# Performance work log

Measured on AMD Instinct MI355X. Metric: run time of the kernel, lower is better.

## Reference

```python
import jax, jax.numpy as jnp
import numpy as np

L1 = 513          # max_data_length + 1
EMB = 64          # embedding_dim (w)
V = 6             # num_tokens
B = 128           # batch

def setup_inputs() -> dict:
    key = jax.random.key(0)
    k1, k2, k3 = jax.random.split(key, 3)
    src = jax.random.randint(k1, (B, L1), 0, V, dtype=jnp.int64)
    # nn.Embedding default init: N(0,1)
    embedding = jax.random.normal(k2, (V, EMB), dtype=jnp.float32)
    # xavier_uniform over (L1, EMB, L1, V): fan_in = EMB*L1*V? torch treats dim0 as fan_out... use gain scale ~ sqrt(6/(fan_in+fan_out)) with fan computed on flattened dims
    fan_in = EMB * L1 * V
    fan_out = L1
    bound = float(np.sqrt(6.0 / (fan_in + fan_out)))
    weight = jax.random.uniform(k3, (L1, EMB, L1, V), dtype=jnp.float32, minval=-bound, maxval=bound)
    bias = jnp.zeros((L1, V), dtype=jnp.float32)
    return {"src": src, "embedding": embedding, "weight": weight, "bias": bias}

def reference(src, embedding, weight, bias):
    # embedding lookup: (B, L1, EMB)
    x = embedding[src].astype(jnp.float32)
    # causal mask over (s, t): lower-triangular ones
    mask = jnp.tril(jnp.ones((L1, L1), dtype=jnp.float32))
    # batched masked trilinear contraction -> (B, L1, V)
    out = jnp.einsum('bsw,swtv,st->btv', x, weight, mask)
    out = out + bias[None, :, :]
    # permute to (B, V, L1)
    return jnp.transpose(out, (0, 2, 1))
```

## Files before the change

### kernel.cpp

```cpp
#include <hip/hip_runtime.h>
#include <hip/hip_bf16.h>

#define L1C 513
#define EMBC 64
#define VC 6
#define BC 128
#define NCOLS (L1C * VC)
#define NTC 64
#define NTILES ((NCOLS + NTC - 1) / NTC)

#define XELEMS ((size_t)L1C * BC * EMBC)
#define XBYTES (XELEMS * 2)
#define OUTELEMS ((size_t)BC * NCOLS)
#define PARTBYTES (OUTELEMS * 2)

typedef __attribute__((ext_vector_type(8))) short short8;
typedef __attribute__((ext_vector_type(4))) float f32x4;

__device__ __forceinline__ unsigned int pack_bf16x2(float a, float b) {
    __hip_bfloat16 ha = __float2bfloat16(a);
    __hip_bfloat16 hb = __float2bfloat16(b);
    unsigned short ua, ub;
    __builtin_memcpy(&ua, &ha, 2);
    __builtin_memcpy(&ub, &hb, 2);
    return (unsigned int)ua | ((unsigned int)ub << 16);
}

__device__ __forceinline__ unsigned short bf16bits(float a) {
    __hip_bfloat16 h = __float2bfloat16(a);
    unsigned short u;
    __builtin_memcpy(&u, &h, 2);
    return u;
}

__global__ void init_out_kernel(float* __restrict__ out, const float* __restrict__ bias) {
    int i = blockIdx.x * 256 + threadIdx.x;
    if (i >= (int)OUTELEMS) return;
    int r = i % NCOLS;
    int v = r / L1C;
    int t = r - v * L1C;
    out[i] = bias[t * VC + v];
}

__global__ void build_x_kernel(const int* __restrict__ src, const float* __restrict__ emb,
                               unsigned short* __restrict__ X) {
    const int s = blockIdx.x;
    const int b = threadIdx.x >> 1;
    const int half = threadIdx.x & 1;
    const int tok = src[b * L1C + s];
    const float2* e = (const float2*)(emb + tok * EMBC + half * 32);
    unsigned int* row = (unsigned int*)(X + ((size_t)s * BC + b) * EMBC) + half * 16;
#pragma unroll
    for (int i = 0; i < 16; ++i) {
        float2 f = e[i];
        row[i] = pack_bf16x2(f.x, f.y);
    }
}

template <bool PARTIAL>
__global__ __launch_bounds__(256) void gemm_tril_kernel(
    const float* __restrict__ Wt, const unsigned short* __restrict__ X,
    void* __restrict__ outp, int CS) {
    const int tile = blockIdx.x;
    const int chunk = blockIdx.y;
    const int n0 = tile * NTC;
    const int s0 = chunk * CS;
    const int sEnd = min(s0 + CS, L1C);

    __shared__ __align__(16) unsigned short Blds[2][NTC * EMBC];

    const int tid = threadIdx.x;
    const int wid = tid >> 6;
    const int lane = tid & 63;
    const int l15 = lane & 15;
    const int h = lane >> 4;

    const int n = n0 + lane;
    const int tcol = n / VC;
    const size_t nsafe = (n < NCOLS) ? (size_t)n : (size_t)(NCOLS - 1);
    const int wrow0 = wid * 16;
    const int wswz = (lane & 7) << 4;

    f32x4 acc[2][4];
#pragma unroll
    for (int i = 0; i < 2; ++i)
#pragma unroll
        for (int j = 0; j < 4; ++j) acc[i][j] = f32x4{0.f, 0.f, 0.f, 0.f};

    const int sBeg = max(s0, n0 / VC);

#define SYNCB()                                                \
    {                                                          \
        __builtin_amdgcn_sched_barrier(0);                     \
        asm volatile("s_waitcnt lgkmcnt(0)" ::: "memory");     \
        __builtin_amdgcn_s_barrier();                          \
        __builtin_amdgcn_sched_barrier(0);                     \
    }

#define ISSUEW(ss, farr)                                                         \
    {                                                                            \
        const int scl_ = ((ss) < L1C) ? (ss) : (L1C - 1);                        \
        const float* wb_ = Wt + ((size_t)scl_ * EMBC + wrow0) * NCOLS + nsafe;   \
        _Pragma("unroll") for (int u_ = 0; u_ < 16; ++u_)                        \
            farr[u_] = wb_[(size_t)u_ * NCOLS];                                  \
    }

#define PACKW(ss, farr, buf)                                                     \
    {                                                                            \
        const bool act_ = (tcol <= (ss));                                        \
        char* dr_ = (char*)Blds[buf] + lane * 128;                               \
        _Pragma("unroll") for (int u_ = 0; u_ < 4; ++u_) {                       \
            float g0 = act_ ? farr[u_ * 4 + 0] : 0.f;                            \
            float g1 = act_ ? farr[u_ * 4 + 1] : 0.f;                            \
            float g2 = act_ ? farr[u_ * 4 + 2] : 0.f;                            \
            float g3 = act_ ? farr[u_ * 4 + 3] : 0.f;                            \
            uint2 pk_ = make_uint2(pack_bf16x2(g0, g1), pack_bf16x2(g2, g3));    \
            *(uint2*)(dr_ + ((2 * (wrow0 + u_ * 4)) ^ wswz)) = pk_;              \
        }                                                                        \
    }

#define ISSUEA(ss, aarr)                                                             \
    {                                                                                \
        const int scl_ = ((ss) < L1C) ? (ss) : (L1C - 1);                            \
        const unsigned short* xr_ = X + (size_t)scl_ * (BC * EMBC);                  \
        aarr[0] = *(const short8*)(xr_ + (wid * 32 + l15) * EMBC + h * 8);           \
        aarr[1] = *(const short8*)(xr_ + (wid * 32 + l15) * EMBC + 32 + h * 8);      \
        aarr[2] = *(const short8*)(xr_ + (wid * 32 + 16 + l15) * EMBC + h * 8);      \
        aarr[3] = *(const short8*)(xr_ + (wid * 32 + 16 + l15) * EMBC + 32 + h * 8); \
    }

#define MFMASTEP(aarr, buf)                                                                              \
    {                                                                                                    \
        _Pragma("unroll") for (int kk_ = 0; kk_ < 2; ++kk_) {                                            \
            const int foff_ = (kk_ * 64 + h * 16) ^ ((l15 & 7) << 4);                                    \
            _Pragma("unroll") for (int nt_ = 0; nt_ < 4; ++nt_) {                                        \
                short8 bb_ = *(const short8*)((const char*)Blds[buf] + (nt_ * 16 + l15) * 128 + foff_);  \
                acc[0][nt_] = __builtin_amdgcn_mfma_f32_16x16x32_bf16(aarr[kk_], bb_, acc[0][nt_], 0, 0, 0);     \
                acc[1][nt_] = __builtin_amdgcn_mfma_f32_16x16x32_bf16(aarr[2 + kk_], bb_, acc[1][nt_], 0, 0, 0); \
            }                                                                                            \
        }                                                                                                \
    }

    if (sBeg < sEnd) {
        float fW0[16], fW1[16];
        short8 aC[4], aN[4];
        ISSUEW(sBeg, fW1);
        PACKW(sBeg, fW1, 0);
        ISSUEW(sBeg + 1, fW0);
        ISSUEA(sBeg, aC);
        SYNCB();

        int s = sBeg, cur = 0;
        while (true) {
            ISSUEW(s + 2, fW1);
            ISSUEA(s + 1, aN);
            MFMASTEP(aC, cur);
            PACKW(s + 1, fW0, cur ^ 1);
            SYNCB();
            cur ^= 1;
            if (++s >= sEnd) break;

            ISSUEW(s + 2, fW0);
            ISSUEA(s + 1, aC);
            MFMASTEP(aN, cur);
            PACKW(s + 1, fW1, cur ^ 1);
            SYNCB();
            cur ^= 1;
            if (++s >= sEnd) break;
        }
    }

#pragma unroll
    for (int nt = 0; nt < 4; ++nt) {
        const int nn = n0 + nt * 16 + l15;
        if (nn >= NCOLS) continue;
        if (PARTIAL) {
            unsigned short* dst = (unsigned short*)outp + (size_t)chunk * OUTELEMS;
#pragma unroll
            for (int ms = 0; ms < 2; ++ms)
#pragma unroll
                for (int r = 0; r < 4; ++r) {
                    const int bi = wid * 32 + ms * 16 + h * 4 + r;
                    dst[(size_t)bi * NCOLS + nn] = bf16bits(acc[ms][nt][r]);
                }
        } else {
            float* dst = (float*)outp;
            const int t = nn / VC;
            const int v = nn - t * VC;
            const size_t obase = (size_t)v * L1C + t;
#pragma unroll
            for (int ms = 0; ms < 2; ++ms)
#pragma unroll
                for (int r = 0; r < 4; ++r) {
                    const int bi = wid * 32 + ms * 16 + h * 4 + r;
                    atomicAdd(dst + (size_t)bi * NCOLS + obase, acc[ms][nt][r]);
                }
        }
    }
#undef SYNCB
#undef ISSUEW
#undef PACKW
#undef ISSUEA
#undef MFMASTEP
}

__global__ void reduce_kernel(const unsigned short* __restrict__ partial,
                              const float* __restrict__ bias,
                              float* __restrict__ out, int nchunks) {
    int i4 = blockIdx.x * 256 + threadIdx.x;
    if (i4 >= (int)(OUTELEMS / 4)) return;
    const size_t base = (size_t)i4 * 4;
    float sum[4];
#pragma unroll
    for (int j = 0; j < 4; ++j) {
        int idx = (int)base + j;
        sum[j] = bias[idx % NCOLS];
    }
    for (int c = 0; c < nchunks; ++c) {
        const ushort4 p = *(const ushort4*)(partial + (size_t)c * OUTELEMS + base);
        unsigned int u0 = (unsigned int)p.x << 16, u1 = (unsigned int)p.y << 16;
        unsigned int u2 = (unsigned int)p.z << 16, u3 = (unsigned int)p.w << 16;
        float f0, f1, f2, f3;
        __builtin_memcpy(&f0, &u0, 4);
        __builtin_memcpy(&f1, &u1, 4);
        __builtin_memcpy(&f2, &u2, 4);
        __builtin_memcpy(&f3, &u3, 4);
        sum[0] += f0;
        sum[1] += f1;
        sum[2] += f2;
        sum[3] += f3;
    }
#pragma unroll
    for (int j = 0; j < 4; ++j) {
        int idx = (int)base + j;
        int b = idx / NCOLS;
        int nn = idx - b * NCOLS;
        int t = nn / VC;
        int v = nn - t * VC;
        out[(size_t)b * NCOLS + (size_t)v * L1C + t] = sum[j];
    }
}

extern "C" void kernel_launch(void* const* d_in, const int* in_sizes, int n_in,
                              void* d_out, int out_size, void* d_ws, size_t ws_size,
                              hipStream_t stream) {
    const int* src = (const int*)d_in[0];
    const float* emb = (const float*)d_in[1];
    const float* wt = (const float*)d_in[2];
    const float* bias = (const float*)d_in[3];
    float* out = (float*)d_out;
    unsigned short* X = (unsigned short*)d_ws;

    build_x_kernel<<<L1C, 256, 0, stream>>>(src, emb, X);

    size_t avail = (ws_size > XBYTES) ? (ws_size - XBYTES) : 0;
    int nchunks = (int)(avail / PARTBYTES);
    if (nchunks > 31) nchunks = 31;

    if (nchunks >= 2) {
        int CS = (L1C + nchunks - 1) / nchunks;
        nchunks = (L1C + CS - 1) / CS;
        unsigned short* partial = (unsigned short*)((char*)d_ws + XBYTES);
        dim3 grid(NTILES, nchunks);
        gemm_tril_kernel<true><<<grid, 256, 0, stream>>>(wt, X, (void*)partial, CS);
        reduce_kernel<<<(int)((OUTELEMS / 4 + 255) / 256), 256, 0, stream>>>(partial, bias, out, nchunks);
    } else {
        init_out_kernel<<<(int)((OUTELEMS + 255) / 256), 256, 0, stream>>>(out, bias);
        dim3 grid(NTILES, 17);
        gemm_tril_kernel<false><<<grid, 256, 0, stream>>>(wt, X, (void*)out, 31);
    }
}
```

Baseline: 93.99 us.

## Widen column tile, vectorize weight loads, fix chunking, skip empty chunks in reduce

```diff
diff --git a/kernel.cpp b/kernel.cpp
--- a/kernel.cpp
+++ b/kernel.cpp
@@ -6,8 +6,10 @@
 #define VC 6
 #define BC 128
 #define NCOLS (L1C * VC)
-#define NTC 64
+#define NTC 128
 #define NTILES ((NCOLS + NTC - 1) / NTC)
+#define CSC 10
+#define NCHUNK ((L1C + CSC - 1) / CSC)
 
 #define XELEMS ((size_t)L1C * BC * EMBC)
 #define XBYTES (XELEMS * 2)
@@ -58,7 +60,7 @@
 }
 
 template <bool PARTIAL>
-__global__ __launch_bounds__(256) void gemm_tril_kernel(
+__global__ __launch_bounds__(256, 3) void gemm_tril_kernel(
     const float* __restrict__ Wt, const unsigned short* __restrict__ X,
     void* __restrict__ outp, int CS) {
     const int tile = blockIdx.x;
@@ -66,6 +68,8 @@
     const int n0 = tile * NTC;
     const int s0 = chunk * CS;
     const int sEnd = min(s0 + CS, L1C);
+    const int sBeg = max(s0, n0 / VC);
+    if (sBeg >= sEnd) return;
 
     __shared__ __align__(16) unsigned short Blds[2][NTC * EMBC];
 
@@ -75,19 +79,18 @@
     const int l15 = lane & 15;
     const int h = lane >> 4;
 
-    const int n = n0 + lane;
-    const int tcol = n / VC;
-    const size_t nsafe = (n < NCOLS) ? (size_t)n : (size_t)(NCOLS - 1);
-    const int wrow0 = wid * 16;
-    const int wswz = (lane & 7) << 4;
-
-    f32x4 acc[2][4];
+    const int colg = (lane & 31) * 4;
+    const int wr0 = wid * 16 + (lane >> 5) * 8;
+    const int c0 = n0 + colg;
+    int tc[4];
+#pragma unroll
+    for (int j = 0; j < 4; ++j) tc[j] = (c0 + j) / VC;
+
+    f32x4 acc[2][8];
 #pragma unroll
     for (int i = 0; i < 2; ++i)
 #pragma unroll
-        for (int j = 0; j < 4; ++j) acc[i][j] = f32x4{0.f, 0.f, 0.f, 0.f};
-
-    const int sBeg = max(s0, n0 / VC);
+        for (int j = 0; j < 8; ++j) acc[i][j] = f32x4{0.f, 0.f, 0.f, 0.f};
 
 #define SYNCB()                                                \
     {                                                          \
@@ -97,26 +100,39 @@
         __builtin_amdgcn_sched_barrier(0);                     \
     }
 
-#define ISSUEW(ss, farr)                                                         \
-    {                                                                            \
-        const int scl_ = ((ss) < L1C) ? (ss) : (L1C - 1);                        \
-        const float* wb_ = Wt + ((size_t)scl_ * EMBC + wrow0) * NCOLS + nsafe;   \
-        _Pragma("unroll") for (int u_ = 0; u_ < 16; ++u_)                        \
-            farr[u_] = wb_[(size_t)u_ * NCOLS];                                  \
-    }
-
-#define PACKW(ss, farr, buf)                                                     \
-    {                                                                            \
-        const bool act_ = (tcol <= (ss));                                        \
-        char* dr_ = (char*)Blds[buf] + lane * 128;                               \
-        _Pragma("unroll") for (int u_ = 0; u_ < 4; ++u_) {                       \
-            float g0 = act_ ? farr[u_ * 4 + 0] : 0.f;                            \
-            float g1 = act_ ? farr[u_ * 4 + 1] : 0.f;                            \
-            float g2 = act_ ? farr[u_ * 4 + 2] : 0.f;                            \
-            float g3 = act_ ? farr[u_ * 4 + 3] : 0.f;                            \
-            uint2 pk_ = make_uint2(pack_bf16x2(g0, g1), pack_bf16x2(g2, g3));    \
-            *(uint2*)(dr_ + ((2 * (wrow0 + u_ * 4)) ^ wswz)) = pk_;              \
-        }                                                                        \
+#define ISSUEW(ss)                                                          \
+    {                                                                       \
+        const int scl_ = ((ss) < L1C) ? (ss) : (L1C - 1);                   \
+        const float* wb_ = Wt + (size_t)(scl_ * EMBC + wr0) * NCOLS;        \
+        if (c0 + 4 <= NCOLS) {                                              \
+            _Pragma("unroll") for (int i_ = 0; i_ < 8; ++i_)                \
+                __builtin_memcpy(&fw[i_], wb_ + (size_t)i_ * NCOLS + c0, 16); \
+        } else {                                                            \
+            _Pragma("unroll") for (int i_ = 0; i_ < 8; ++i_) {              \
+                _Pragma("unroll") for (int j_ = 0; j_ < 4; ++j_) {          \
+                    const int cj_ = (c0 + j_ < NCOLS) ? (c0 + j_) : (NCOLS - 1); \
+                    fw[i_][j_] = wb_[(size_t)i_ * NCOLS + cj_];             \
+                }                                                           \
+            }                                                               \
+        }                                                                   \
+    }
+
+#define PACKW(ss, buf)                                                      \
+    {                                                                       \
+        _Pragma("unroll") for (int j_ = 0; j_ < 4; ++j_) {                  \
+            const bool act_ = (tc[j_] <= (ss));                             \
+            const int cl_ = colg + j_;                                      \
+            char* dr_ = (char*)Blds[buf] + cl_ * 128;                       \
+            const int sw_ = (cl_ & 7) << 4;                                 \
+            _Pragma("unroll") for (int u_ = 0; u_ < 2; ++u_) {              \
+                float g0 = act_ ? fw[u_ * 4 + 0][j_] : 0.f;                 \
+                float g1 = act_ ? fw[u_ * 4 + 1][j_] : 0.f;                 \
+                float g2 = act_ ? fw[u_ * 4 + 2][j_] : 0.f;                 \
+                float g3 = act_ ? fw[u_ * 4 + 3][j_] : 0.f;                 \
+                uint2 pk_ = make_uint2(pack_bf16x2(g0, g1), pack_bf16x2(g2, g3)); \
+                *(uint2*)(dr_ + ((2 * (wr0 + 4 * u_)) ^ sw_)) = pk_;        \
+            }                                                               \
+        }                                                                   \
     }
 
 #define ISSUEA(ss, aarr)                                                             \
@@ -133,7 +149,7 @@
     {                                                                                                    \
         _Pragma("unroll") for (int kk_ = 0; kk_ < 2; ++kk_) {                                            \
             const int foff_ = (kk_ * 64 + h * 16) ^ ((l15 & 7) << 4);                                    \
-            _Pragma("unroll") for (int nt_ = 0; nt_ < 4; ++nt_) {                                        \
+            _Pragma("unroll") for (int nt_ = 0; nt_ < 8; ++nt_) {                                        \
                 short8 bb_ = *(const short8*)((const char*)Blds[buf] + (nt_ * 16 + l15) * 128 + foff_);  \
                 acc[0][nt_] = __builtin_amdgcn_mfma_f32_16x16x32_bf16(aarr[kk_], bb_, acc[0][nt_], 0, 0, 0);     \
                 acc[1][nt_] = __builtin_amdgcn_mfma_f32_16x16x32_bf16(aarr[2 + kk_], bb_, acc[1][nt_], 0, 0, 0); \
@@ -141,29 +157,28 @@
         }                                                                                                \
     }
 
-    if (sBeg < sEnd) {
-        float fW0[16], fW1[16];
+    {
+        f32x4 fw[8];
         short8 aC[4], aN[4];
-        ISSUEW(sBeg, fW1);
-        PACKW(sBeg, fW1, 0);
-        ISSUEW(sBeg + 1, fW0);
+        ISSUEW(sBeg);
+        PACKW(sBeg, 0);
         ISSUEA(sBeg, aC);
         SYNCB();
 
         int s = sBeg, cur = 0;
         while (true) {
-            ISSUEW(s + 2, fW1);
+            ISSUEW(s + 1);
             ISSUEA(s + 1, aN);
             MFMASTEP(aC, cur);
-            PACKW(s + 1, fW0, cur ^ 1);
+            PACKW(s + 1, cur ^ 1);
             SYNCB();
             cur ^= 1;
             if (++s >= sEnd) break;
 
-            ISSUEW(s + 2, fW0);
+            ISSUEW(s + 1);
             ISSUEA(s + 1, aC);
             MFMASTEP(aN, cur);
-            PACKW(s + 1, fW1, cur ^ 1);
+            PACKW(s + 1, cur ^ 1);
             SYNCB();
             cur ^= 1;
             if (++s >= sEnd) break;
@@ -171,7 +186,7 @@
     }
 
 #pragma unroll
-    for (int nt = 0; nt < 4; ++nt) {
+    for (int nt = 0; nt < 8; ++nt) {
         const int nn = n0 + nt * 16 + l15;
         if (nn >= NCOLS) continue;
         if (PARTIAL) {
@@ -206,17 +221,24 @@
 
 __global__ void reduce_kernel(const unsigned short* __restrict__ partial,
                               const float* __restrict__ bias,
-                              float* __restrict__ out, int nchunks) {
+                              float* __restrict__ out, int nchunks, int CS) {
     int i4 = blockIdx.x * 256 + threadIdx.x;
     if (i4 >= (int)(OUTELEMS / 4)) return;
     const size_t base = (size_t)i4 * 4;
     float sum[4];
+    int cf[4];
+    int cmin = 1 << 30;
 #pragma unroll
     for (int j = 0; j < 4; ++j) {
         int idx = (int)base + j;
-        sum[j] = bias[idx % NCOLS];
-    }
-    for (int c = 0; c < nchunks; ++c) {
+        int nn = idx % NCOLS;
+        sum[j] = bias[nn];
+        int tl = nn >> 7;
+        int tmin = (tl << 7) / VC;
+        cf[j] = tmin / CS;
+        cmin = min(cmin, cf[j]);
+    }
+    for (int c = cmin; c < nchunks; ++c) {
         const ushort4 p = *(const ushort4*)(partial + (size_t)c * OUTELEMS + base);
         unsigned int u0 = (unsigned int)p.x << 16, u1 = (unsigned int)p.y << 16;
         unsigned int u2 = (unsigned int)p.z << 16, u3 = (unsigned int)p.w << 16;
@@ -225,10 +247,10 @@
         __builtin_memcpy(&f1, &u1, 4);
         __builtin_memcpy(&f2, &u2, 4);
         __builtin_memcpy(&f3, &u3, 4);
-        sum[0] += f0;
-        sum[1] += f1;
-        sum[2] += f2;
-        sum[3] += f3;
+        if (c >= cf[0]) sum[0] += f0;
+        if (c >= cf[1]) sum[1] += f1;
+        if (c >= cf[2]) sum[2] += f2;
+        if (c >= cf[3]) sum[3] += f3;
     }
 #pragma unroll
     for (int j = 0; j < 4; ++j) {
@@ -253,17 +275,11 @@
 
     build_x_kernel<<<L1C, 256, 0, stream>>>(src, emb, X);
 
-    size_t avail = (ws_size > XBYTES) ? (ws_size - XBYTES) : 0;
-    int nchunks = (int)(avail / PARTBYTES);
-    if (nchunks > 31) nchunks = 31;
-
-    if (nchunks >= 2) {
-        int CS = (L1C + nchunks - 1) / nchunks;
-        nchunks = (L1C + CS - 1) / CS;
+    if (ws_size >= XBYTES + (size_t)NCHUNK * PARTBYTES) {
         unsigned short* partial = (unsigned short*)((char*)d_ws + XBYTES);
-        dim3 grid(NTILES, nchunks);
-        gemm_tril_kernel<true><<<grid, 256, 0, stream>>>(wt, X, (void*)partial, CS);
-        reduce_kernel<<<(int)((OUTELEMS / 4 + 255) / 256), 256, 0, stream>>>(partial, bias, out, nchunks);
+        dim3 grid(NTILES, NCHUNK);
+        gemm_tril_kernel<true><<<grid, 256, 0, stream>>>(wt, X, (void*)partial, CSC);
+        reduce_kernel<<<(int)((OUTELEMS / 4 + 255) / 256), 256, 0, stream>>>(partial, bias, out, NCHUNK, CSC);
     } else {
         init_out_kernel<<<(int)((OUTELEMS + 255) / 256), 256, 0, stream>>>(out, bias);
         dim3 grid(NTILES, 17);
```

Result: slower. 100.6 us (+7.1%).
